# Optimization experiments

Hardware: AMD Instinct MI355X
Metric: run time of the kernel (lower is better)

Reference implementation:

```python
import jax, jax.numpy as jnp
import numpy as np

N_ATOM = 30000
N_PAIR = 1_000_000
N_TRI = 4_000_000
N_SF = 16
RC = 6.0

LAMBD = jnp.array([-1.0, 1.0] * 8, dtype=jnp.float32)
ZETA = jnp.array([1.0, 1.0, 2.0, 2.0, 4.0, 4.0, 8.0, 8.0] * 2, dtype=jnp.float32)
ETA = jnp.array([0.01, 0.014, 0.02, 0.028, 0.04, 0.056, 0.08, 0.11,
                 0.16, 0.22, 0.32, 0.45, 0.63, 0.72, 0.9, 1.0], dtype=jnp.float32)


def cutoff_f1(r):
    # PiNN 'f1' cutoff: 0.5*(cos(pi*r/rc)+1)
    return 0.5 * (jnp.cos(jnp.float32(np.pi) * r / RC) + 1.0)


def gaussian_basis(r, fc):
    # GaussianBasis with center=0, gamma=eta: fc * exp(-eta * r^2), shape [n, n_sf]
    return fc[:, None] * jnp.exp(-ETA[None, :] * (r[:, None] ** 2))


def setup_inputs() -> dict:
    key = jax.random.key(0)
    k1, k2, k3, k4, k5 = jax.random.split(key, 5)
    ind_2 = jax.random.randint(k1, (N_PAIR, 2), 0, N_ATOM, dtype=jnp.int32)
    ind_3 = jax.random.randint(k2, (N_TRI, 2), 0, N_PAIR, dtype=jnp.int32)
    dist = jax.random.uniform(k3, (N_PAIR,), jnp.float32, 0.5, RC)
    dirs = jax.random.normal(k4, (N_PAIR, 3), jnp.float32)
    dirs = dirs / jnp.linalg.norm(dirs, axis=1, keepdims=True)
    diff = dirs * dist[:, None]  # bond vectors consistent with dist
    elems = jax.random.randint(k5, (N_ATOM,), 0, 4, dtype=jnp.int32)
    fc = cutoff_f1(dist)
    return {"ind_2": ind_2, "ind_3": ind_3, "dist": dist, "diff": diff,
            "elems": elems, "fc": fc}


def reference(ind_2, ind_3, dist, diff, elems, fc):
    # i=j=k='ALL': species filter is identity; a_rind = arange(n_atom)
    ind_ij = ind_3[:, 0]
    ind_ik = ind_3[:, 1]
    i_rind = ind_2[ind_ij, 0]  # central atom index per triplet

    diff_ij = diff[ind_ij]  # [T,3]
    diff_ik = diff[ind_ik]
    diff_jk = diff_ik - diff_ij
    dist_jk = jnp.linalg.norm(diff_jk, axis=1)
    mask = dist_jk < RC  # TF filters triplets; we mask (jit-friendly)

    fc_jk = cutoff_f1(dist_jk)
    dist_ij = dist[ind_ij]
    dist_ik = dist[ind_ik]
    fc_ij = fc[ind_ij]
    fc_ik = fc[ind_ik]

    cos_ijk = jnp.einsum('id,id->i', diff_ij, diff_ik) / dist_ij / dist_ik
    base = jnp.maximum(1.0 + LAMBD[None, :] * cos_ijk[:, None], 0.0)
    sf = (2.0 ** (1.0 - ZETA[None, :]) * base ** ZETA[None, :]
          * gaussian_basis(dist_ij, fc_ij)
          * gaussian_basis(dist_ik, fc_ik)
          * gaussian_basis(dist_jk, fc_jk))
    sf = jnp.where(mask[:, None], sf, 0.0)

    # scatter_nd add into per-atom fingerprints
    fp = jnp.zeros((N_ATOM, N_SF), dtype=sf.dtype).at[i_rind].add(sf)

    # jacobian indices: central-atom rel index per participating pair
    vals = jnp.where(mask, i_rind, -1)
    seg = jnp.concatenate([ind_ij, ind_ik])
    pair_i = jax.ops.segment_max(jnp.concatenate([vals, vals]), seg,
                                 num_segments=N_PAIR)
    pair_i = jnp.maximum(pair_i, -1)  # empty segments -> -1 sentinel
    jacob_ind = jnp.stack([jnp.arange(N_PAIR, dtype=jnp.int32), pair_i], axis=1)
    return fp, jacob_ind
```

## Files before the change

### kernel.cpp

```cpp
#include <hip/hip_runtime.h>

#define N_ATOM 30000
#define N_PAIR 1000000
#define N_TRI  4000000
#define N_SF   16
#define FP_ELEMS (N_ATOM * N_SF)

#define ASH  5
#define APB  32
#define NCB  938
#define NSUB 8
#define NSEG (NCB * NSUB)
#define OVF_CNT_IDX NSEG
#define OVF_CAP 131072
#define TILE 4096
#define PER_TH 16
#define NTILES ((N_TRI + TILE - 1) / TILE)

#define OFF_CCNT  0ULL
#define OFF_IKMAX 65536ULL
#define OFF_AOFP  4065536ULL
#define OFF_FLAG  6065536ULL
#define OFF_OVF   7065536ULL
#define OFF_PACK  8114112ULL
#define OFF_CB    24114112ULL

__device__ __constant__ float c_eta[16] = {
    0.01f, 0.014f, 0.02f, 0.028f, 0.04f, 0.056f, 0.08f, 0.11f,
    0.16f, 0.22f, 0.32f, 0.45f, 0.63f, 0.72f, 0.9f, 1.0f};

__device__ __forceinline__ bool tri_math_pack(
    float4 A, float4 B, float A8[8], float& R2)
{
    float ax = A.x, ay = A.y, az = A.z, fcij = A.w;
    float bx = B.x, by = B.y, bz = B.z, fcik = B.w;
    float d2ij = fmaf(ax, ax, fmaf(ay, ay, az * az));
    float d2ik = fmaf(bx, bx, fmaf(by, by, bz * bz));
    float jx = bx - ax, jy = by - ay, jz = bz - az;
    float d2jk = fmaf(jx, jx, fmaf(jy, jy, jz * jz));
    if (!(d2jk < 36.0f)) return false;
    float dij = sqrtf(d2ij);
    float dik = sqrtf(d2ik);
    float djk = sqrtf(d2jk);
    const float PI_OVER_RC = 0.5235987755982988f;
    float fcjk = 0.5f * (__cosf(PI_OVER_RC * djk) + 1.0f);
    float dot = fmaf(ax, bx, fmaf(ay, by, az * bz));
    float cosv = dot / (dij * dik);
    R2 = d2ij + d2ik + d2jk;
    float FCt = fcij * fcik * fcjk;
    float bm = fmaxf(1.0f - cosv, 0.0f);
    float bp = fmaxf(1.0f + cosv, 0.0f);
    float bm2 = bm * bm, bp2 = bp * bp;
    float bm4 = bm2 * bm2, bp4 = bp2 * bp2;
    float bm8 = bm4 * bm4, bp8 = bp4 * bp4;
    A8[0] = FCt * bm;              A8[1] = FCt * bp;
    A8[2] = 0.5f * FCt * bm2;      A8[3] = 0.5f * FCt * bp2;
    A8[4] = 0.125f * FCt * bm4;    A8[5] = 0.125f * FCt * bp4;
    A8[6] = 0.0078125f * FCt * bm8; A8[7] = 0.0078125f * FCt * bp8;
    return true;
}


__global__ __launch_bounds__(256) void prep2(
    const int2* __restrict__ ind2, const float* __restrict__ diff,
    const float* __restrict__ fc,
    int* __restrict__ ccnt, int* __restrict__ ikmax,
    unsigned short* __restrict__ aofp, unsigned char* __restrict__ flag,
    float4* __restrict__ pack, float* __restrict__ out)
{
    int p = blockIdx.x * blockDim.x + threadIdx.x;
    if (p <= NSEG) ccnt[p] = 0;
    if (p < FP_ELEMS) out[p] = 0.0f;
    if (p >= N_PAIR) return;
    ikmax[p] = -1;
    flag[p] = 0;
    aofp[p] = (unsigned short)ind2[p].x;
    float4 r;
    r.x = diff[3 * p + 0];
    r.y = diff[3 * p + 1];
    r.z = diff[3 * p + 2];
    r.w = fc[p];
    pack[p] = r;
}

__global__ __launch_bounds__(256) void bin3(
    const int2* __restrict__ ind3, const unsigned short* __restrict__ aofp,
    int* __restrict__ ccnt, int2* __restrict__ cbucket,
    int2* __restrict__ ovf, int cap)
{
    __shared__ int lcnt[NCB];
    __shared__ int lbase[NCB];
    const int thr = threadIdx.x;
    const int sub = blockIdx.x & (NSUB - 1);
    const long long t0 = (long long)blockIdx.x * TILE;

    for (int i = thr; i < NCB; i += 256) lcnt[i] = 0;
    __syncthreads();

    int myatom[PER_TH];
    int myslot[PER_TH];
#pragma unroll
    for (int j = 0; j < PER_TH; ++j) {
        long long t = t0 + j * 256 + thr;
        int a = 0, s = -1;
        if (t < N_TRI) {
            int ij = ind3[t].x;
            a = aofp[ij];
            s = atomicAdd(&lcnt[a >> ASH], 1);
        }
        myatom[j] = a;
        myslot[j] = s;
    }
    __syncthreads();
    for (int c = thr; c < NCB; c += 256) {
        int n = lcnt[c];
        lbase[c] = n ? atomicAdd(&ccnt[c * NSUB + sub], n) : 0;
    }
    __syncthreads();
#pragma unroll
    for (int j = 0; j < PER_TH; ++j) {
        long long t = t0 + j * 256 + thr;
        if (t >= N_TRI) continue;
        int a = myatom[j];
        int c = a >> ASH;
        int slot = lbase[c] + myslot[j];
        int2 pr = ind3[t];
        if (slot < cap) {
            int2 e;
            e.x = pr.x | ((a & (APB - 1)) << 20);
            e.y = pr.y;
            cbucket[(size_t)(c * NSUB + sub) * cap + slot] = e;
        } else {
            int o = atomicAdd(&ccnt[OVF_CNT_IDX], 1);
            if (o < OVF_CAP) ovf[o] = pr;
        }
    }
}

__global__ __launch_bounds__(256) void reduce4(
    const int* __restrict__ ccnt, const int2* __restrict__ cbucket, int cap,
    const float4* __restrict__ pack,
    int* __restrict__ ikmax, unsigned char* __restrict__ flag,
    float* __restrict__ out)
{
    __shared__ float lacc[APB * 17];
    const int seg = blockIdx.x;
    const int b = seg >> 3;
    const int thr = threadIdx.x;
    for (int i = thr; i < APB * 17; i += 256) lacc[i] = 0.0f;
    __syncthreads();

    int n = ccnt[seg];
    n = min(n, cap);
    const int2* segp = cbucket + (size_t)seg * cap;
    for (int i = thr; i < n; i += 256) {
        int2 e = segp[i];
        int a5 = (e.x >> 20) & (APB - 1);
        int ij = e.x & 0xFFFFF;
        int ik = e.y;
        float4 A = pack[ij];
        float4 B = pack[ik];
        float A8[8], R2;
        if (!tri_math_pack(A, B, A8, R2)) continue;
        flag[ij] = 1;
        atomicMax(&ikmax[ik], (b << ASH) + a5);
#pragma unroll
        for (int s = 0; s < 16; ++s)
            atomicAdd(&lacc[a5 * 17 + s], A8[s & 7] * __expf(-c_eta[s] * R2));
    }
    __syncthreads();
    for (int t = thr; t < APB * N_SF; t += 256) {
        int atom = (b << ASH) + (t >> 4);
        float v = lacc[(t >> 4) * 17 + (t & 15)];
        if (atom < N_ATOM && v != 0.0f)
            unsafeAtomicAdd(out + (size_t)atom * N_SF + (t & 15), v);
    }
}

__global__ __launch_bounds__(256) void ovf3(
    const int* __restrict__ ccnt, const int2* __restrict__ ovf,
    const float4* __restrict__ pack, const unsigned short* __restrict__ aofp,
    int* __restrict__ ikmax, unsigned char* __restrict__ flag,
    float* __restrict__ out)
{
    int i = blockIdx.x * blockDim.x + threadIdx.x;
    int n = ccnt[OVF_CNT_IDX];
    if (n > OVF_CAP) n = OVF_CAP;
    if (i >= n) return;
    int2 pr = ovf[i];
    int ij = pr.x, ik = pr.y;
    float A8[8], R2;
    if (!tri_math_pack(pack[ij], pack[ik], A8, R2)) return;
    int atom = aofp[ij];
    flag[ij] = 1;
    atomicMax(&ikmax[ik], atom);
    float* base = out + (size_t)atom * N_SF;
#pragma unroll
    for (int s = 0; s < 16; ++s)
        unsafeAtomicAdd(base + s, A8[s & 7] * __expf(-c_eta[s] * R2));
}

__global__ __launch_bounds__(256) void fin3(
    const int* __restrict__ ikmax, const unsigned char* __restrict__ flag,
    const unsigned short* __restrict__ aofp, float* __restrict__ out)
{
    int p = blockIdx.x * blockDim.x + threadIdx.x;
    if (p >= N_PAIR) return;
    int v = ikmax[p];
    if (flag[p]) { int a = aofp[p]; v = v > a ? v : a; }
    float* jf = out + FP_ELEMS;
    jf[2 * p + 0] = (float)p;
    jf[2 * p + 1] = (float)v;
}


__global__ __launch_bounds__(256) void init_legacy(float* __restrict__ out) {
    int i = blockIdx.x * blockDim.x + threadIdx.x;
    if (i < FP_ELEMS) out[i] = 0.0f;
    if (i < N_PAIR) ((int*)out + FP_ELEMS)[2 * i + 1] = -1;
}

__global__ __launch_bounds__(256) void tri_legacy(
    const int* __restrict__ ind2, const int2* __restrict__ ind3,
    const float* __restrict__ dist, const float* __restrict__ diff,
    const float* __restrict__ fc, float* __restrict__ out) {
    int t = blockIdx.x * blockDim.x + threadIdx.x;
    if (t >= N_TRI) return;
    int2 pr = ind3[t];
    int ij = pr.x, ik = pr.y;
    float4 A, B;
    A.x = diff[3 * ij + 0]; A.y = diff[3 * ij + 1]; A.z = diff[3 * ij + 2]; A.w = fc[ij];
    B.x = diff[3 * ik + 0]; B.y = diff[3 * ik + 1]; B.z = diff[3 * ik + 2]; B.w = fc[ik];
    float A8[8], R2;
    if (!tri_math_pack(A, B, A8, R2)) return;
    int atom = ind2[2 * ij];
    int* jac = (int*)out + FP_ELEMS;
    atomicMax(&jac[2 * ij + 1], atom);
    atomicMax(&jac[2 * ik + 1], atom);
    float* base = out + (size_t)atom * N_SF;
#pragma unroll
    for (int s = 0; s < 16; ++s)
        unsafeAtomicAdd(base + s, A8[s & 7] * __expf(-c_eta[s] * R2));
}

__global__ __launch_bounds__(256) void fin_legacy(float* __restrict__ out) {
    int p = blockIdx.x * blockDim.x + threadIdx.x;
    if (p >= N_PAIR) return;
    int* jac = (int*)out + FP_ELEMS;
    int v = jac[2 * p + 1];
    float* jf = (float*)jac;
    jf[2 * p + 0] = (float)p;
    jf[2 * p + 1] = (float)v;
}


extern "C" void kernel_launch(void* const* d_in, const int* in_sizes, int n_in,
                              void* d_out, int out_size, void* d_ws, size_t ws_size,
                              hipStream_t stream) {
    const int2*  ind2 = (const int2*)d_in[0];
    const int2*  ind3 = (const int2*)d_in[1];
    const float* dist = (const float*)d_in[2];
    const float* diff = (const float*)d_in[3];
    const float* fc   = (const float*)d_in[5];
    float* out = (float*)d_out;

    const size_t seg_stride = (size_t)NSEG * sizeof(int2);
    const size_t need_min = OFF_CB + seg_stride * 608;

    if (ws_size >= need_min) {
        char* ws = (char*)d_ws;
        int* ccnt            = (int*)(ws + OFF_CCNT);
        int* ikmax           = (int*)(ws + OFF_IKMAX);
        unsigned short* aofp = (unsigned short*)(ws + OFF_AOFP);
        unsigned char* flag  = (unsigned char*)(ws + OFF_FLAG);
        int2* ovf            = (int2*)(ws + OFF_OVF);
        float4* pack         = (float4*)(ws + OFF_PACK);
        int2* cbucket        = (int2*)(ws + OFF_CB);
        int cap = (int)((ws_size - OFF_CB) / seg_stride);
        if (cap > 1024) cap = 1024;

        int pb = (N_PAIR + 255) / 256;
        prep2<<<pb, 256, 0, stream>>>(ind2, diff, fc, ccnt, ikmax, aofp, flag, pack, out);
        bin3<<<NTILES, 256, 0, stream>>>(ind3, aofp, ccnt, cbucket, ovf, cap);
        reduce4<<<NSEG, 256, 0, stream>>>(ccnt, cbucket, cap, pack, ikmax, flag, out);
        ovf3<<<OVF_CAP / 256, 256, 0, stream>>>(ccnt, ovf, pack, aofp, ikmax, flag, out);
        fin3<<<pb, 256, 0, stream>>>(ikmax, flag, aofp, out);
    } else {
        init_legacy<<<(N_PAIR + 255) / 256, 256, 0, stream>>>(out);
        tri_legacy<<<(N_PAIR * 4 + 255) / 256, 256, 0, stream>>>((const int*)d_in[0], ind3, dist, diff, fc, out);
        fin_legacy<<<(N_PAIR + 255) / 256, 256, 0, stream>>>(out);
    }
}
```

Measured before the change: 445.7 us.

## Sort pair data by central-atom chunk and stage ij packs in shared memory

Pairs are now counting-sorted by central-atom chunk (histogram, scan, placement), so each reduce block can load its chunk's ij pair vectors into an LDS window instead of gathering them from global memory. The per-pair max of the central atom is stored in the w lane of the packed float4, replacing the separate ikmax/flag/aofp arrays, and fc is recomputed from distance instead of loaded. bin3 now also gathers the amap for ik and resolves its sorted position, which adds an extra random read. The change also adds three small pre-pass kernels and more global atomics in the placement step.

```diff
diff --git a/kernel.cpp b/kernel.cpp
--- a/kernel.cpp
+++ b/kernel.cpp
@@ -16,24 +16,27 @@
 #define TILE 4096
 #define PER_TH 16
 #define NTILES ((N_TRI + TILE - 1) / TILE)
-
-#define OFF_CCNT  0ULL
-#define OFF_IKMAX 65536ULL
-#define OFF_AOFP  4065536ULL
-#define OFF_FLAG  6065536ULL
-#define OFF_OVF   7065536ULL
-#define OFF_PACK  8114112ULL
-#define OFF_CB    24114112ULL
+#define WCAP 1280
+
+#define OFF_CCNT   0ULL
+#define OFF_PCNT   32768ULL
+#define OFF_PPLACE 98304ULL
+#define OFF_PBASE  163840ULL
+#define OFF_AMAP   196608ULL
+#define OFF_OVF    4196608ULL
+#define OFF_PACKS  5245184ULL
+#define OFF_CB     21245184ULL
+#define ZERO_INTS  41984
 
 __device__ __constant__ float c_eta[16] = {
     0.01f, 0.014f, 0.02f, 0.028f, 0.04f, 0.056f, 0.08f, 0.11f,
     0.16f, 0.22f, 0.32f, 0.45f, 0.63f, 0.72f, 0.9f, 1.0f};
 
-__device__ __forceinline__ bool tri_math_pack(
+__device__ __forceinline__ bool tri_math(
     float4 A, float4 B, float A8[8], float& R2)
 {
-    float ax = A.x, ay = A.y, az = A.z, fcij = A.w;
-    float bx = B.x, by = B.y, bz = B.z, fcik = B.w;
+    float ax = A.x, ay = A.y, az = A.z;
+    float bx = B.x, by = B.y, bz = B.z;
     float d2ij = fmaf(ax, ax, fmaf(ay, ay, az * az));
     float d2ik = fmaf(bx, bx, fmaf(by, by, bz * bz));
     float jx = bx - ax, jy = by - ay, jz = bz - az;
@@ -43,6 +46,8 @@
     float dik = sqrtf(d2ik);
     float djk = sqrtf(d2jk);
     const float PI_OVER_RC = 0.5235987755982988f;
+    float fcij = 0.5f * (__cosf(PI_OVER_RC * dij) + 1.0f);
+    float fcik = 0.5f * (__cosf(PI_OVER_RC * dik) + 1.0f);
     float fcjk = 0.5f * (__cosf(PI_OVER_RC * djk) + 1.0f);
     float dot = fmaf(ax, bx, fmaf(ay, by, az * bz));
     float cosv = dot / (dij * dik);
@@ -53,38 +58,80 @@
     float bm2 = bm * bm, bp2 = bp * bp;
     float bm4 = bm2 * bm2, bp4 = bp2 * bp2;
     float bm8 = bm4 * bm4, bp8 = bp4 * bp4;
-    A8[0] = FCt * bm;              A8[1] = FCt * bp;
-    A8[2] = 0.5f * FCt * bm2;      A8[3] = 0.5f * FCt * bp2;
-    A8[4] = 0.125f * FCt * bm4;    A8[5] = 0.125f * FCt * bp4;
+    A8[0] = FCt * bm;               A8[1] = FCt * bp;
+    A8[2] = 0.5f * FCt * bm2;       A8[3] = 0.5f * FCt * bp2;
+    A8[4] = 0.125f * FCt * bm4;     A8[5] = 0.125f * FCt * bp4;
     A8[6] = 0.0078125f * FCt * bm8; A8[7] = 0.0078125f * FCt * bp8;
     return true;
 }
 
 
-__global__ __launch_bounds__(256) void prep2(
+__global__ __launch_bounds__(256) void zero_meta(int* __restrict__ m)
+{
+    int i = blockIdx.x * blockDim.x + threadIdx.x;
+    if (i < ZERO_INTS) m[i] = 0;
+}
+
+__global__ __launch_bounds__(256) void pair_hist(
+    const int2* __restrict__ ind2, int* __restrict__ pcnt)
+{
+    __shared__ int h[NCB];
+    for (int i = threadIdx.x; i < NCB; i += 256) h[i] = 0;
+    __syncthreads();
+    int stride = gridDim.x * 256;
+    for (int p = blockIdx.x * 256 + threadIdx.x; p < N_PAIR; p += stride)
+        atomicAdd(&h[ind2[p].x >> ASH], 1);
+    __syncthreads();
+    for (int i = threadIdx.x; i < NCB; i += 256) {
+        int v = h[i];
+        if (v) atomicAdd(&pcnt[i * 16], v);
+    }
+}
+
+__global__ __launch_bounds__(1024) void scan_bases(
+    const int* __restrict__ pcnt, int* __restrict__ pbase)
+{
+    __shared__ int s[1024];
+    int t = threadIdx.x;
+    int v0 = (t < NCB) ? pcnt[t * 16] : 0;
+    s[t] = v0;
+    __syncthreads();
+    for (int off = 1; off < 1024; off <<= 1) {
+        int v = 0;
+        if (t >= off) v = s[t - off];
+        __syncthreads();
+        s[t] += v;
+        __syncthreads();
+    }
+    if (t < NCB) pbase[t] = s[t] - v0;
+    if (t == 0) pbase[NCB] = N_PAIR;
+}
+
+__global__ __launch_bounds__(256) void pair_place(
     const int2* __restrict__ ind2, const float* __restrict__ diff,
-    const float* __restrict__ fc,
-    int* __restrict__ ccnt, int* __restrict__ ikmax,
-    unsigned short* __restrict__ aofp, unsigned char* __restrict__ flag,
-    float4* __restrict__ pack, float* __restrict__ out)
+    const int* __restrict__ pbase, int* __restrict__ pplace,
+    unsigned int* __restrict__ amap, float4* __restrict__ packs,
+    float* __restrict__ out)
 {
     int p = blockIdx.x * blockDim.x + threadIdx.x;
-    if (p <= NSEG) ccnt[p] = 0;
     if (p < FP_ELEMS) out[p] = 0.0f;
     if (p >= N_PAIR) return;
-    ikmax[p] = -1;
-    flag[p] = 0;
-    aofp[p] = (unsigned short)ind2[p].x;
+    int a = ind2[p].x;
+    int c = a >> ASH;
+    int l = atomicAdd(&pplace[c * 16], 1);
+    int q = pbase[c] + l;
+    amap[p] = ((unsigned)c << 22) | ((unsigned)(a & (APB - 1)) << 17) | (unsigned)l;
     float4 r;
     r.x = diff[3 * p + 0];
     r.y = diff[3 * p + 1];
     r.z = diff[3 * p + 2];
-    r.w = fc[p];
-    pack[p] = r;
+    r.w = __int_as_float(-1);
+    packs[q] = r;
 }
 
 __global__ __launch_bounds__(256) void bin3(
-    const int2* __restrict__ ind3, const unsigned short* __restrict__ aofp,
+    const int2* __restrict__ ind3, const unsigned int* __restrict__ amap,
+    const int* __restrict__ pbase,
     int* __restrict__ ccnt, int2* __restrict__ cbucket,
     int2* __restrict__ ovf, int cap)
 {
@@ -97,19 +144,21 @@
     for (int i = thr; i < NCB; i += 256) lcnt[i] = 0;
     __syncthreads();
 
-    int myatom[PER_TH];
-    int myslot[PER_TH];
+    unsigned int mij_r[PER_TH];
+    int qik_r[PER_TH];
+    int slot_r[PER_TH];
 #pragma unroll
     for (int j = 0; j < PER_TH; ++j) {
         long long t = t0 + j * 256 + thr;
-        int a = 0, s = -1;
+        unsigned int mij = 0; int qik = 0, s = -1;
         if (t < N_TRI) {
-            int ij = ind3[t].x;
-            a = aofp[ij];
-            s = atomicAdd(&lcnt[a >> ASH], 1);
+            int2 pr = ind3[t];
+            mij = amap[pr.x];
+            unsigned int mik = amap[pr.y];
+            qik = pbase[mik >> 22] + (int)(mik & 0x1FFFF);
+            s = atomicAdd(&lcnt[mij >> 22], 1);
         }
-        myatom[j] = a;
-        myslot[j] = s;
+        mij_r[j] = mij; qik_r[j] = qik; slot_r[j] = s;
     }
     __syncthreads();
     for (int c = thr; c < NCB; c += 256) {
@@ -121,49 +170,54 @@
     for (int j = 0; j < PER_TH; ++j) {
         long long t = t0 + j * 256 + thr;
         if (t >= N_TRI) continue;
-        int a = myatom[j];
-        int c = a >> ASH;
-        int slot = lbase[c] + myslot[j];
-        int2 pr = ind3[t];
+        unsigned int mij = mij_r[j];
+        int c = mij >> 22;
+        int slot = lbase[c] + slot_r[j];
         if (slot < cap) {
             int2 e;
-            e.x = pr.x | ((a & (APB - 1)) << 20);
-            e.y = pr.y;
+            e.x = (int)(mij & 0x3FFFFF);
+            e.y = qik_r[j];
             cbucket[(size_t)(c * NSUB + sub) * cap + slot] = e;
         } else {
             int o = atomicAdd(&ccnt[OVF_CNT_IDX], 1);
-            if (o < OVF_CAP) ovf[o] = pr;
+            if (o < OVF_CAP) { int2 e; e.x = (int)mij; e.y = qik_r[j]; ovf[o] = e; }
         }
     }
 }
 
 __global__ __launch_bounds__(256) void reduce4(
     const int* __restrict__ ccnt, const int2* __restrict__ cbucket, int cap,
-    const float4* __restrict__ pack,
-    int* __restrict__ ikmax, unsigned char* __restrict__ flag,
+    float4* __restrict__ packs, const int* __restrict__ pbase,
     float* __restrict__ out)
 {
+    __shared__ float4 win[WCAP];
     __shared__ float lacc[APB * 17];
     const int seg = blockIdx.x;
     const int b = seg >> 3;
     const int thr = threadIdx.x;
+    const int base = pbase[b];
+    const int wlen = min(pbase[b + 1] - base, WCAP);
+
     for (int i = thr; i < APB * 17; i += 256) lacc[i] = 0.0f;
+    for (int i = thr; i < wlen; i += 256) win[i] = packs[base + i];
     __syncthreads();
 
     int n = ccnt[seg];
     n = min(n, cap);
     const int2* segp = cbucket + (size_t)seg * cap;
+    int* pw = (int*)packs;
     for (int i = thr; i < n; i += 256) {
         int2 e = segp[i];
-        int a5 = (e.x >> 20) & (APB - 1);
-        int ij = e.x & 0xFFFFF;
-        int ik = e.y;
-        float4 A = pack[ij];
-        float4 B = pack[ik];
+        int lidx = e.x & 0x1FFFF;
+        int a5 = (e.x >> 17) & (APB - 1);
+        int qik = e.y;
+        float4 A = (lidx < wlen) ? win[lidx] : packs[base + lidx];
+        float4 B = packs[qik];
         float A8[8], R2;
-        if (!tri_math_pack(A, B, A8, R2)) continue;
-        flag[ij] = 1;
-        atomicMax(&ikmax[ik], (b << ASH) + a5);
+        if (!tri_math(A, B, A8, R2)) continue;
+        int atom = (b << ASH) + a5;
+        atomicMax(&pw[4 * (base + lidx) + 3], atom);
+        atomicMax(&pw[4 * qik + 3], atom);
 #pragma unroll
         for (int s = 0; s < 16; ++s)
             atomicAdd(&lacc[a5 * 17 + s], A8[s & 7] * __expf(-c_eta[s] * R2));
@@ -179,35 +233,43 @@
 
 __global__ __launch_bounds__(256) void ovf3(
     const int* __restrict__ ccnt, const int2* __restrict__ ovf,
-    const float4* __restrict__ pack, const unsigned short* __restrict__ aofp,
-    int* __restrict__ ikmax, unsigned char* __restrict__ flag,
+    float4* __restrict__ packs, const int* __restrict__ pbase,
     float* __restrict__ out)
 {
     int i = blockIdx.x * blockDim.x + threadIdx.x;
     int n = ccnt[OVF_CNT_IDX];
     if (n > OVF_CAP) n = OVF_CAP;
     if (i >= n) return;
-    int2 pr = ovf[i];
-    int ij = pr.x, ik = pr.y;
+    int2 e = ovf[i];
+    unsigned int mij = (unsigned int)e.x;
+    int qik = e.y;
+    int c = mij >> 22;
+    int a5 = (mij >> 17) & (APB - 1);
+    int lidx = mij & 0x1FFFF;
+    int qij = pbase[c] + lidx;
+    float4 A = packs[qij];
+    float4 B = packs[qik];
     float A8[8], R2;
-    if (!tri_math_pack(pack[ij], pack[ik], A8, R2)) return;
-    int atom = aofp[ij];
-    flag[ij] = 1;
-    atomicMax(&ikmax[ik], atom);
-    float* base = out + (size_t)atom * N_SF;
+    if (!tri_math(A, B, A8, R2)) return;
+    int atom = (c << ASH) + a5;
+    int* pw = (int*)packs;
+    atomicMax(&pw[4 * qij + 3], atom);
+    atomicMax(&pw[4 * qik + 3], atom);
+    float* basep = out + (size_t)atom * N_SF;
 #pragma unroll
     for (int s = 0; s < 16; ++s)
-        unsafeAtomicAdd(base + s, A8[s & 7] * __expf(-c_eta[s] * R2));
+        unsafeAtomicAdd(basep + s, A8[s & 7] * __expf(-c_eta[s] * R2));
 }
 
 __global__ __launch_bounds__(256) void fin3(
-    const int* __restrict__ ikmax, const unsigned char* __restrict__ flag,
-    const unsigned short* __restrict__ aofp, float* __restrict__ out)
+    const unsigned int* __restrict__ amap, const int* __restrict__ pbase,
+    const float4* __restrict__ packs, float* __restrict__ out)
 {
     int p = blockIdx.x * blockDim.x + threadIdx.x;
     if (p >= N_PAIR) return;
-    int v = ikmax[p];
-    if (flag[p]) { int a = aofp[p]; v = v > a ? v : a; }
+    unsigned int m = amap[p];
+    int q = pbase[m >> 22] + (int)(m & 0x1FFFF);
+    int v = ((const int*)packs)[4 * q + 3];
     float* jf = out + FP_ELEMS;
     jf[2 * p + 0] = (float)p;
     jf[2 * p + 1] = (float)v;
@@ -229,10 +291,10 @@
     int2 pr = ind3[t];
     int ij = pr.x, ik = pr.y;
     float4 A, B;
-    A.x = diff[3 * ij + 0]; A.y = diff[3 * ij + 1]; A.z = diff[3 * ij + 2]; A.w = fc[ij];
-    B.x = diff[3 * ik + 0]; B.y = diff[3 * ik + 1]; B.z = diff[3 * ik + 2]; B.w = fc[ik];
+    A.x = diff[3 * ij + 0]; A.y = diff[3 * ij + 1]; A.z = diff[3 * ij + 2]; A.w = 0.f;
+    B.x = diff[3 * ik + 0]; B.y = diff[3 * ik + 1]; B.z = diff[3 * ik + 2]; B.w = 0.f;
     float A8[8], R2;
-    if (!tri_math_pack(A, B, A8, R2)) return;
+    if (!tri_math(A, B, A8, R2)) return;
     int atom = ind2[2 * ij];
     int* jac = (int*)out + FP_ELEMS;
     atomicMax(&jac[2 * ij + 1], atom);
@@ -270,24 +332,29 @@
     if (ws_size >= need_min) {
         char* ws = (char*)d_ws;
         int* ccnt            = (int*)(ws + OFF_CCNT);
-        int* ikmax           = (int*)(ws + OFF_IKMAX);
-        unsigned short* aofp = (unsigned short*)(ws + OFF_AOFP);
-        unsigned char* flag  = (unsigned char*)(ws + OFF_FLAG);
+        int* pcnt            = (int*)(ws + OFF_PCNT);
+        int* pplace          = (int*)(ws + OFF_PPLACE);
+        int* pbase           = (int*)(ws + OFF_PBASE);
+        unsigned int* amap   = (unsigned int*)(ws + OFF_AMAP);
         int2* ovf            = (int2*)(ws + OFF_OVF);
-        float4* pack         = (float4*)(ws + OFF_PACK);
+        float4* packs        = (float4*)(ws + OFF_PACKS);
         int2* cbucket        = (int2*)(ws + OFF_CB);
         int cap = (int)((ws_size - OFF_CB) / seg_stride);
         if (cap > 1024) cap = 1024;
 
         int pb = (N_PAIR + 255) / 256;
-        prep2<<<pb, 256, 0, stream>>>(ind2, diff, fc, ccnt, ikmax, aofp, flag, pack, out);
-        bin3<<<NTILES, 256, 0, stream>>>(ind3, aofp, ccnt, cbucket, ovf, cap);
-        reduce4<<<NSEG, 256, 0, stream>>>(ccnt, cbucket, cap, pack, ikmax, flag, out);
-        ovf3<<<OVF_CAP / 256, 256, 0, stream>>>(ccnt, ovf, pack, aofp, ikmax, flag, out);
-        fin3<<<pb, 256, 0, stream>>>(ikmax, flag, aofp, out);
+        zero_meta<<<(ZERO_INTS + 255) / 256, 256, 0, stream>>>((int*)ws);
+        pair_hist<<<240, 256, 0, stream>>>(ind2, pcnt);
+        scan_bases<<<1, 1024, 0, stream>>>(pcnt, pbase);
+        pair_place<<<pb, 256, 0, stream>>>(ind2, diff, pbase, pplace, amap, packs, out);
+        bin3<<<NTILES, 256, 0, stream>>>(ind3, amap, pbase, ccnt, cbucket, ovf, cap);
+        reduce4<<<NSEG, 256, 0, stream>>>(ccnt, cbucket, cap, packs, pbase, out);
+        ovf3<<<OVF_CAP / 256, 256, 0, stream>>>(ccnt, ovf, packs, pbase, out);
+        fin3<<<pb, 256, 0, stream>>>(amap, pbase, packs, out);
     } else {
         init_legacy<<<(N_PAIR + 255) / 256, 256, 0, stream>>>(out);
-        tri_legacy<<<(N_PAIR * 4 + 255) / 256, 256, 0, stream>>>((const int*)d_in[0], ind3, dist, diff, fc, out);
+        tri_legacy<<<(N_TRI + 255) / 256, 256, 0, stream>>>((const int*)d_in[0], ind3, dist, diff, fc, out);
         fin_legacy<<<(N_PAIR + 255) / 256, 256, 0, stream>>>(out);
     }
-}
+    (void)dist; (void)fc; (void)in_sizes; (void)n_in; (void)out_size;
+}
```

Result: slower. 539.0 us (+20.9%).
